# Optimization experiments

Hardware: AMD Instinct MI355X
Metric: run time of the kernel (lower is better)

The kernel has to match this reference:

```python
import jax, jax.numpy as jnp
import numpy as np

YOLO_INPUT_SIZE = 416.0
SCORE_THRESHOLD = 0.5
IOU_THRESHOLD = 0.45
AREA_THRESHOLD = 0.0005
MAX_OUTPUT_BOXES = 10
NEG = -1e9


def setup_inputs() -> dict:
    key = jax.random.key(0)
    y = jax.random.uniform(key, (64, 10647, 85), dtype=jnp.float32)
    # first 4 channels are xywh in input-pixel units (YOLO decode divides by 416)
    y = y.at[..., 0:2].multiply(YOLO_INPUT_SIZE)          # centers in [0, 416)
    y = y.at[..., 2:4].multiply(YOLO_INPUT_SIZE * 0.3)    # w,h up to ~125 px
    return {"y_pred": y}


def _decode(y_pred):
    flat = y_pred.reshape(-1, y_pred.shape[-1])           # [N, 85]
    box, conf, probs = flat[:, :4], flat[:, 4], flat[:, 5:]
    scores = conf * jnp.max(probs, axis=-1)               # [N]
    classes = jnp.argmax(probs, axis=-1).astype(jnp.int32)
    b = jnp.clip(box / YOLO_INPUT_SIZE, 0.0, 1.0)
    x, y, w, h = b[:, 0], b[:, 1], b[:, 2], b[:, 3]
    x1 = jnp.clip(x - w * 0.5, 0.0, 1.0)
    y1 = jnp.clip(y - h * 0.5, 0.0, 1.0)
    x2 = jnp.clip(x + w * 0.5, 0.0, 1.0)
    y2 = jnp.clip(y + h * 0.5, 0.0, 1.0)
    big_enough = (x2 - x1) * (y2 - y1) > AREA_THRESHOLD
    keep = big_enough & (scores > SCORE_THRESHOLD)
    boxes = jnp.stack([x1, y1, x2, y2], axis=-1)          # [N, 4]
    work = jnp.where(keep, scores, NEG)                   # masked working scores
    return boxes, scores, classes, work


def _iou_one_vs_all(ref, boxes):
    ix1 = jnp.maximum(ref[0], boxes[:, 0])
    iy1 = jnp.maximum(ref[1], boxes[:, 1])
    ix2 = jnp.minimum(ref[2], boxes[:, 2])
    iy2 = jnp.minimum(ref[3], boxes[:, 3])
    inter = jnp.maximum(ix2 - ix1, 0.0) * jnp.maximum(iy2 - iy1, 0.0)
    a_ref = (ref[2] - ref[0]) * (ref[3] - ref[1])
    a_all = (boxes[:, 2] - boxes[:, 0]) * (boxes[:, 3] - boxes[:, 1])
    return inter / (a_ref + a_all - inter + 1e-10)


def _greedy_nms(boxes, work):
    def step(w, _):
        j = jnp.argmax(w)
        v = w[j] > SCORE_THRESHOLD
        iou = _iou_one_vs_all(boxes[j], boxes)
        w = jnp.where(v & (iou > IOU_THRESHOLD), NEG, w)
        w = w.at[j].set(NEG)
        return w, (j.astype(jnp.int32), v)
    _, (idxs, valid) = jax.lax.scan(step, work, None, length=MAX_OUTPUT_BOXES)
    return idxs, valid


def reference(y_pred):
    boxes, scores, classes, work = _decode(y_pred)
    idxs, valid = _greedy_nms(boxes, work)
    # fixed-size (padded) outputs instead of dynamic boolean gather; `valid`
    # marks real detections (original returns only the valid rows)
    sel_boxes = boxes[idxs]                # [10, 4]
    sel_scores = scores[idxs][:, None]     # [10, 1]
    sel_classes = classes[idxs][:, None]   # [10, 1]
    return sel_boxes, sel_scores, sel_classes, valid
```

## Files before the change

kernel.cpp:

```cpp
#include <hip/hip_runtime.h>

#define ROWS   681408
#define NBINS  8192
#define CAP    64
#define TOPK   192
#define SELCAP 256

#define WS_ROW0     4
#define WS_CNT      16
#define WS_BUCKET   8448

__device__ __forceinline__ float clip01(float v) {
    return fminf(fmaxf(v, 0.0f), 1.0f);
}

__global__ void init_kernel(unsigned int* __restrict__ ws) {
    int i = blockIdx.x * 256 + threadIdx.x;
    if (i < NBINS) ws[WS_CNT + i] = 0u;
}

__global__ __launch_bounds__(256) void decode_kernel(
    const float* __restrict__ y, unsigned int* __restrict__ ws)
{
    const int t    = threadIdx.x;
    const int lane = t & 63;
    const int wave = t >> 6;
    const int s    = lane & 3;
    const int qr   = lane >> 2;
    const int row  = blockIdx.x * 64 + wave * 16 + qr;

    const float*  p  = y + (size_t)row * 85;
    const float4* p4 = (const float4*)p;

    float4 f0 = p4[s];
    float4 f1 = p4[s + 4];
    float4 f2 = p4[s + 8];
    float4 f3 = p4[s + 12];
    float4 f4v = p4[s + 16];
    float4 ft = make_float4(-1.0f, -1.0f, -1.0f, -1.0f);
    float e84 = -1.0f;
    if (s == 0) ft = p4[20];
    if (s == 1) e84 = p[84];

    float bv = -1.0f; int bc = 1 << 20;
    {
        const int b0 = 4 * s;
        if (b0 + 0 >= 5 && f0.x > bv) { bv = f0.x; bc = b0 - 5; }
        if (b0 + 1 >= 5 && f0.y > bv) { bv = f0.y; bc = b0 - 4; }
        if (b0 + 2 >= 5 && f0.z > bv) { bv = f0.z; bc = b0 - 3; }
        if (b0 + 3 >= 5 && f0.w > bv) { bv = f0.w; bc = b0 - 2; }
        if (f1.x > bv) { bv = f1.x; bc = b0 + 11; }
        if (f1.y > bv) { bv = f1.y; bc = b0 + 12; }
        if (f1.z > bv) { bv = f1.z; bc = b0 + 13; }
        if (f1.w > bv) { bv = f1.w; bc = b0 + 14; }
        if (f2.x > bv) { bv = f2.x; bc = b0 + 27; }
        if (f2.y > bv) { bv = f2.y; bc = b0 + 28; }
        if (f2.z > bv) { bv = f2.z; bc = b0 + 29; }
        if (f2.w > bv) { bv = f2.w; bc = b0 + 30; }
        if (f3.x > bv) { bv = f3.x; bc = b0 + 43; }
        if (f3.y > bv) { bv = f3.y; bc = b0 + 44; }
        if (f3.z > bv) { bv = f3.z; bc = b0 + 45; }
        if (f3.w > bv) { bv = f3.w; bc = b0 + 46; }
        if (f4v.x > bv) { bv = f4v.x; bc = b0 + 59; }
        if (f4v.y > bv) { bv = f4v.y; bc = b0 + 60; }
        if (f4v.z > bv) { bv = f4v.z; bc = b0 + 61; }
        if (f4v.w > bv) { bv = f4v.w; bc = b0 + 62; }
        if (s == 0) {
            if (ft.x > bv) { bv = ft.x; bc = 75; }
            if (ft.y > bv) { bv = ft.y; bc = 76; }
            if (ft.z > bv) { bv = ft.z; bc = 77; }
            if (ft.w > bv) { bv = ft.w; bc = 78; }
        }
        if (s == 1 && e84 > bv) { bv = e84; bc = 79; }
    }

    #pragma unroll
    for (int m = 1; m <= 2; m <<= 1) {
        float ov = __shfl_xor(bv, m, 64);
        int   oc = __shfl_xor(bc, m, 64);
        if (ov > bv || (ov == bv && oc < bc)) { bv = ov; bc = oc; }
    }

    float cf = __shfl(f0.x, (lane & 60) + 1, 64);

    if (s == 0) {
        float score = cf * bv;
        float x  = clip01(f0.x / 416.0f);
        float yy = clip01(f0.y / 416.0f);
        float w  = clip01(f0.z / 416.0f);
        float h  = clip01(f0.w / 416.0f);
        float x1 = clip01(x  - w * 0.5f);
        float y1 = clip01(yy - h * 0.5f);
        float x2 = clip01(x  + w * 0.5f);
        float y2 = clip01(yy + h * 0.5f);
        bool keep = (((x2 - x1) * (y2 - y1)) > 0.0005f) && (score > 0.5f);
        if (keep) {
            int bin = (int)((score - 0.5f) * (2.0f * (float)NBINS));
            bin = min(max(bin, 0), NBINS - 1);
            unsigned int pos = atomicAdd(&ws[WS_CNT + bin], 1u);
            if (pos < (unsigned int)CAP) {
                uint2* bucket = (uint2*)&ws[WS_BUCKET];
                bucket[bin * CAP + pos] =
                    make_uint2(__float_as_uint(score), (unsigned int)row);
            }
        }
        if (row == 0) {
            float* r0 = (float*)&ws[WS_ROW0];
            r0[0] = score; r0[1] = (float)bc;
            r0[2] = x1; r0[3] = y1; r0[4] = x2; r0[5] = y2;
        }
    }
}

__global__ __launch_bounds__(256) void nms_kernel(
    const float* __restrict__ y, unsigned int* __restrict__ ws,
    float* __restrict__ out)
{
    __shared__ unsigned int chunk[256];
    __shared__ unsigned int fine[32];
    __shared__ unsigned long long keys[SELCAP];
    __shared__ float4 sboxes[SELCAP];
    __shared__ int s_coarse;
    __shared__ int s_bstar;
    __shared__ unsigned int s_m;
    __shared__ int s_picks;
    __shared__ unsigned int s_idx[10];
    __shared__ float s_score[10];
    __shared__ float4 s_box[10];
    __shared__ int s_cls[10];

    const int t = threadIdx.x;
    const uint2* bucket = (const uint2*)&ws[WS_BUCKET];

    unsigned int ssum = 0;
    {
        const uint4* cnt4 = (const uint4*)&ws[WS_CNT];
        #pragma unroll
        for (int i = 0; i < 8; i++) {
            uint4 v = cnt4[t * 8 + i];
            ssum += min(v.x, (unsigned int)CAP) + min(v.y, (unsigned int)CAP)
                  + min(v.z, (unsigned int)CAP) + min(v.w, (unsigned int)CAP);
        }
    }
    chunk[t] = ssum;
    for (int i = t; i < SELCAP; i += 256) keys[i] = 0ull;
    if (t == 0) s_m = 0u;
    __syncthreads();

    for (int off = 1; off < 256; off <<= 1) {
        unsigned int v = chunk[t];
        unsigned int a = (t + off < 256) ? chunk[t + off] : 0u;
        __syncthreads();
        chunk[t] = v + a;
        __syncthreads();
    }
    const unsigned int total  = chunk[0];
    const unsigned int target = (total < (unsigned int)TOPK) ? total
                                                             : (unsigned int)TOPK;

    if (target > 0) {
        if (chunk[t] >= target && (t == 255 || chunk[t + 1] < target))
            s_coarse = t;
        __syncthreads();

        const int cb = s_coarse * 32;
        if (t < 32) fine[t] = min(ws[WS_CNT + cb + t], (unsigned int)CAP);
        __syncthreads();
        for (int off = 1; off < 32; off <<= 1) {
            unsigned int v = 0, a = 0;
            if (t < 32) { v = fine[t]; a = (t + off < 32) ? fine[t + off] : 0u; }
            __syncthreads();
            if (t < 32) fine[t] = v + a;
            __syncthreads();
        }
        const unsigned int base = (s_coarse < 255) ? chunk[s_coarse + 1] : 0u;
        if (t < 32) {
            unsigned int sfx = base + fine[t];
            unsigned int nxt = (t == 31) ? base : base + fine[t + 1];
            if (sfx >= target && nxt < target) s_bstar = cb + t;
        }
    } else {
        if (t == 0) s_bstar = NBINS;
    }
    __syncthreads();

    for (int bin = s_bstar + t; bin < NBINS; bin += 256) {
        unsigned int c = ws[WS_CNT + bin];
        if (c > (unsigned int)CAP) c = CAP;
        for (unsigned int j = 0; j < c; j++) {
            uint2 cv = bucket[bin * CAP + j];
            unsigned int pos = atomicAdd(&s_m, 1u);
            if (pos < (unsigned int)SELCAP)
                keys[pos] = ((unsigned long long)cv.x << 32) |
                            (unsigned long long)(0xFFFFFFFFu - cv.y);
        }
    }
    __syncthreads();
    unsigned int M = s_m;
    if (M > (unsigned int)SELCAP) M = SELCAP;

    for (int k = 2; k <= SELCAP; k <<= 1) {
        for (int j = k >> 1; j > 0; j >>= 1) {
            for (int i = t; i < SELCAP; i += 256) {
                int ixj = i ^ j;
                if (ixj > i) {
                    unsigned long long a = keys[i], b = keys[ixj];
                    bool descSeg = ((i & k) == 0);
                    if (descSeg ? (a < b) : (a > b)) { keys[i] = b; keys[ixj] = a; }
                }
            }
            __syncthreads();
        }
    }

    for (int i = t; i < (int)M; i += 256) {
        unsigned int idx = 0xFFFFFFFFu - (unsigned int)(keys[i] & 0xFFFFFFFFull);
        const float* p = y + (size_t)idx * 85;
        float x  = clip01(p[0] / 416.0f);
        float yy = clip01(p[1] / 416.0f);
        float w  = clip01(p[2] / 416.0f);
        float h  = clip01(p[3] / 416.0f);
        sboxes[i] = make_float4(clip01(x - w * 0.5f), clip01(yy - h * 0.5f),
                                clip01(x + w * 0.5f), clip01(yy + h * 0.5f));
    }
    __syncthreads();

    if (t == 0) {
        int np = 0;
        for (int i = 0; i < (int)M && np < 10; i++) {
            float4 b = sboxes[i];
            bool ok = true;
            for (int kk = 0; kk < np; kk++) {
                float4 r = s_box[kk];
                float ix1 = fmaxf(r.x, b.x);
                float iy1 = fmaxf(r.y, b.y);
                float ix2 = fminf(r.z, b.z);
                float iy2 = fminf(r.w, b.w);
                float inter = fmaxf(ix2 - ix1, 0.0f) * fmaxf(iy2 - iy1, 0.0f);
                float aref = (r.z - r.x) * (r.w - r.y);
                float aall = (b.z - b.x) * (b.w - b.y);
                float iou = inter / (aref + aall - inter + 1e-10f);
                if (iou > 0.45f) { ok = false; break; }
            }
            if (ok) {
                s_box[np] = b;
                s_idx[np] = 0xFFFFFFFFu - (unsigned int)(keys[i] & 0xFFFFFFFFull);
                s_score[np] = __uint_as_float((unsigned int)(keys[i] >> 32));
                np++;
            }
        }
        s_picks = np;
    }
    __syncthreads();

    {
        int p = t >> 4, s = t & 15;
        float bv = -1.0f; int bc = 1 << 20;
        if (p < s_picks) {
            const float* pr = y + (size_t)s_idx[p] * 85 + 5;
            #pragma unroll
            for (int kk = 0; kk < 5; kk++) {
                float v = pr[s + 16 * kk];
                int c = s + 16 * kk;
                if (v > bv) { bv = v; bc = c; }
            }
        }
        #pragma unroll
        for (int m = 8; m >= 1; m >>= 1) {
            float ov = __shfl_xor(bv, m, 64);
            int   oc = __shfl_xor(bc, m, 64);
            if (ov > bv || (ov == bv && oc < bc)) { bv = ov; bc = oc; }
        }
        if (p < s_picks && s == 0) s_cls[p] = bc;
    }
    __syncthreads();

    if (t == 0) {
        const float* r0 = (const float*)&ws[WS_ROW0];
        float score0 = r0[0], class0 = r0[1];
        float4 box0 = make_float4(r0[2], r0[3], r0[4], r0[5]);
        for (int kk = 0; kk < 10; kk++) {
            bool v = kk < s_picks;
            float4 b = v ? s_box[kk] : box0;
            out[4 * kk + 0] = b.x;
            out[4 * kk + 1] = b.y;
            out[4 * kk + 2] = b.z;
            out[4 * kk + 3] = b.w;
            out[40 + kk] = v ? s_score[kk] : score0;
            out[50 + kk] = v ? (float)s_cls[kk] : class0;
            out[60 + kk] = v ? 1.0f : 0.0f;
        }
    }
}

extern "C" void kernel_launch(void* const* d_in, const int* in_sizes, int n_in,
                              void* d_out, int out_size, void* d_ws, size_t ws_size,
                              hipStream_t stream)
{
    const float* y = (const float*)d_in[0];
    unsigned int* ws = (unsigned int*)d_ws;

    init_kernel<<<dim3(NBINS / 256), dim3(256), 0, stream>>>(ws);
    decode_kernel<<<dim3(ROWS / 64), dim3(256), 0, stream>>>(y, ws);
    nms_kernel<<<dim3(1), dim3(256), 0, stream>>>(y, ws, (float*)d_out);
}
```

Before: 70.40 us.

## Prefilter rows by confidence before full decode via compacted candidate list

Adds a pass that reads only the confidence channel of each row and stream-compacts rows with conf > 0.5 (plus row 0) into a candidate list. The decode kernel then loads the full 85-float row only for those candidates, exiting early on the others. The aim is to cut the global memory traffic of reading every full row, since score = conf*maxprob can only pass the threshold when conf does. The cost is an extra kernel launch, scattered strided reads of the confidence values, an atomic per block, and a decode grid that stays sized for every row.

```diff
diff --git a/kernel.cpp b/kernel.cpp
--- a/kernel.cpp
+++ b/kernel.cpp
@@ -6,9 +6,11 @@
 #define TOPK   192
 #define SELCAP 256
 
+#define WS_NCAND    0
 #define WS_ROW0     4
 #define WS_CNT      16
 #define WS_BUCKET   8448
+#define WS_CAND     1057024
 
 __device__ __forceinline__ float clip01(float v) {
     return fminf(fmaxf(v, 0.0f), 1.0f);
@@ -17,18 +19,73 @@
 __global__ void init_kernel(unsigned int* __restrict__ ws) {
     int i = blockIdx.x * 256 + threadIdx.x;
     if (i < NBINS) ws[WS_CNT + i] = 0u;
-}
-
-__global__ __launch_bounds__(256) void decode_kernel(
-    const float* __restrict__ y, unsigned int* __restrict__ ws)
+    if (i < 4) ws[i] = 0u;
+}
+
+__global__ __launch_bounds__(256) void conf_kernel(
+    const float* __restrict__ y, unsigned int* __restrict__ ws,
+    unsigned int* __restrict__ cand)
 {
+    __shared__ unsigned int wcnt[4];
+    __shared__ unsigned int wbase[4];
+
     const int t    = threadIdx.x;
     const int lane = t & 63;
-    const int wave = t >> 6;
+    const int wv   = t >> 6;
+    const unsigned int base = blockIdx.x * 1024;
+    const unsigned long long below = (1ull << lane) - 1ull;
+
+    unsigned int r[4];
+    bool f[4];
+    unsigned long long m[4];
+    unsigned int c[4];
+
+    #pragma unroll
+    for (int k = 0; k < 4; k++) {
+        r[k] = base + t + 256 * k;
+        bool ok = false;
+        if (r[k] < (unsigned int)ROWS) {
+            float cf = y[(size_t)r[k] * 85 + 4];
+            ok = (cf > 0.5f) || (r[k] == 0);
+        }
+        f[k] = ok;
+        m[k] = __ballot(ok);
+        c[k] = (unsigned int)__popcll(m[k]);
+    }
+
+    if (lane == 0) wcnt[wv] = c[0] + c[1] + c[2] + c[3];
+    __syncthreads();
+    if (t == 0) {
+        unsigned int tot = wcnt[0] + wcnt[1] + wcnt[2] + wcnt[3];
+        unsigned int g = atomicAdd(&ws[WS_NCAND], tot);
+        #pragma unroll
+        for (int w = 0; w < 4; w++) { wbase[w] = g; g += wcnt[w]; }
+    }
+    __syncthreads();
+
+    unsigned int off = wbase[wv];
+    #pragma unroll
+    for (int k = 0; k < 4; k++) {
+        if (f[k])
+            cand[off + (unsigned int)__popcll(m[k] & below)] = r[k];
+        off += c[k];
+    }
+}
+
+__global__ __launch_bounds__(256) void decode_kernel(
+    const float* __restrict__ y, unsigned int* __restrict__ ws,
+    const unsigned int* __restrict__ cand)
+{
+    const unsigned int ncand = ws[WS_NCAND];
+    const int t    = threadIdx.x;
+    const int lane = t & 63;
+    const int wv   = t >> 6;
     const int s    = lane & 3;
     const int qr   = lane >> 2;
-    const int row  = blockIdx.x * 64 + wave * 16 + qr;
-
+    const unsigned int q = blockIdx.x * 64 + wv * 16 + qr;
+    if (q >= ncand) return;
+
+    const unsigned int row = cand[q];
     const float*  p  = y + (size_t)row * 85;
     const float4* p4 = (const float4*)p;
 
@@ -101,7 +158,7 @@
             if (pos < (unsigned int)CAP) {
                 uint2* bucket = (uint2*)&ws[WS_BUCKET];
                 bucket[bin * CAP + pos] =
-                    make_uint2(__float_as_uint(score), (unsigned int)row);
+                    make_uint2(__float_as_uint(score), row);
             }
         }
         if (row == 0) {
@@ -299,8 +356,10 @@
 {
     const float* y = (const float*)d_in[0];
     unsigned int* ws = (unsigned int*)d_ws;
+    unsigned int* cand = ws + WS_CAND;
 
     init_kernel<<<dim3(NBINS / 256), dim3(256), 0, stream>>>(ws);
-    decode_kernel<<<dim3(ROWS / 64), dim3(256), 0, stream>>>(y, ws);
+    conf_kernel<<<dim3((ROWS + 1023) / 1024), dim3(256), 0, stream>>>(y, ws, cand);
+    decode_kernel<<<dim3((ROWS + 63) / 64), dim3(256), 0, stream>>>(y, ws, cand);
     nms_kernel<<<dim3(1), dim3(256), 0, stream>>>(y, ws, (float*)d_out);
 }
```

After: 76.06 us. 8.0% more time.
